# Optimization experiments

Measured on AMD Instinct MI355X. Metric: run time of the kernel, lower is better.

Reference implementation:

```python
import jax, jax.numpy as jnp
import numpy as np

B, N, D, H = 2, 2048, 1024, 16
DH = D // H
SCALE = DH ** -0.5

def setup_inputs() -> dict:
    key = jax.random.key(0)
    k1, k2, k3 = jax.random.split(key, 3)
    x = jax.random.normal(k1, (B, N, D), dtype=jnp.float32)
    W_qkv = jax.random.normal(k2, (3 * D, D), dtype=jnp.float32) * (D ** -0.5)
    W_out = jax.random.normal(k3, (D, D), dtype=jnp.float32) * (D ** -0.5)
    mask = jnp.tril(jnp.ones((N, N), dtype=jnp.int32))  # causal mask; 0 -> -inf
    return {"x": x, "mask": mask, "W_qkv": W_qkv, "W_out": W_out}

def reference(x, mask, W_qkv, W_out):
    b, n, d = x.shape
    qkv = x @ W_qkv.T                                   # [B,N,3D]
    qkv = qkv.reshape(b, n, 3, H, DH).transpose(2, 0, 3, 1, 4)  # [3,B,H,N,DH]
    q, k, v = qkv[0], qkv[1], qkv[2]
    attn = jnp.einsum('bhqd,bhkd->bhqk', q, k) * SCALE  # [B,H,N,N]
    attn = jnp.where(mask == 0, -jnp.inf, attn)
    attn = jax.nn.softmax(attn, axis=-1)
    out = jnp.einsum('bhqk,bhkd->bhqd', attn, v)        # [B,H,N,DH]
    out = out.transpose(0, 2, 1, 3).reshape(b, n, d)    # [B,N,D]
    return out @ W_out.T
```

## Files before the change

### kernel.cpp

```cpp
#include <hip/hip_runtime.h>
#include <hip/hip_bf16.h>


typedef __hip_bfloat16 bf16;
typedef short bf16x8 __attribute__((ext_vector_type(8)));
typedef short bf16x4 __attribute__((ext_vector_type(4)));
typedef float f32x4 __attribute__((ext_vector_type(4)));

#define QSCALE 0.1803368801111204f

typedef __attribute__((address_space(3))) unsigned int lds_u32;
typedef const __attribute__((address_space(1))) unsigned int glob_u32;

__device__ __forceinline__ void glds16(const void* g, void* l) {
    __builtin_amdgcn_global_load_lds((glob_u32*)g, (lds_u32*)l, 16, 0, 0);
}

__device__ __forceinline__ short f2bf(float f) {
    __hip_bfloat16 h = __float2bfloat16(f);
    return *reinterpret_cast<short*>(&h);
}

__device__ __forceinline__ unsigned pack_bf16(float a, float b) {
    unsigned au = __builtin_bit_cast(unsigned, a) + 0x8000u;
    unsigned bu = __builtin_bit_cast(unsigned, b) + 0x8000u;
    return __builtin_amdgcn_perm(bu, au, 0x07060302u);
}

__global__ void cast_all(const float* __restrict__ x, const float* __restrict__ wqkv,
                         const float* __restrict__ wout,
                         bf16* __restrict__ xb, bf16* __restrict__ wqkvb,
                         bf16* __restrict__ woutb) {
    int i = blockIdx.x * blockDim.x + threadIdx.x;
    const float4* s; short4* d; int o;
    if (i < 1048576)               { s = (const float4*)x;    d = (short4*)xb;    o = i; }
    else if (i < 1835008)          { s = (const float4*)wqkv; d = (short4*)wqkvb; o = i - 1048576; }
    else                           { s = (const float4*)wout; d = (short4*)woutb; o = i - 1835008; }
    float4 f = s[o];
    short4 v;
    v.x = f2bf(f.x); v.y = f2bf(f.y); v.z = f2bf(f.z); v.w = f2bf(f.w);
    d[o] = v;
}

__global__ __launch_bounds__(256)
void gemm128_qkv(const bf16* __restrict__ A, const bf16* __restrict__ Bt,
                 bf16* __restrict__ qp, bf16* __restrict__ kp, bf16* __restrict__ vp,
                 int K) {
    __shared__ alignas(16) short As[2][4096];
    __shared__ alignas(16) short Bs[2][4096];

    const int tid = threadIdx.x;
    const int wave = tid >> 6, lane = tid & 63;
    const int quad = lane >> 4, l16 = lane & 15;
    const int wm = wave >> 1, wn = wave & 1;
    const int m0 = blockIdx.x * 128;
    const int n0 = blockIdx.y * 128;

    f32x4 acc[4][4] = {};

    const int srow = tid >> 2;
    const int skk  = (((tid & 3) ^ ((tid >> 3) & 3))) * 8;
    const bf16* Ag = A  + (size_t)(m0 + srow) * K + skk;
    const bf16* Bg = Bt + (size_t)(n0 + srow) * K + skk;
    const size_t rowskip = (size_t)64 * K;
    short* Asl = &As[0][0] + tid * 8;
    short* Bsl = &Bs[0][0] + tid * 8;

    const int xk = (quad ^ ((l16 >> 1) & 3)) * 8;
    const int arow = wm * 64 + l16;
    const int brow = wn * 64 + l16;

    const int KI = K >> 5;
    glds16(Ag, Asl);
    glds16(Ag + rowskip, Asl + 2048);
    glds16(Bg, Bsl);
    glds16(Bg + rowskip, Bsl + 2048);
    __syncthreads();

    int buf = 0;
    for (int ki = 0; ki < KI; ++ki) {
        if (ki + 1 < KI) {
            const bf16* ag = Ag + (ki + 1) * 32;
            const bf16* bg = Bg + (ki + 1) * 32;
            short* ad = Asl + (buf ^ 1) * 4096;
            short* bd = Bsl + (buf ^ 1) * 4096;
            glds16(ag, ad);
            glds16(ag + rowskip, ad + 2048);
            glds16(bg, bd);
            glds16(bg + rowskip, bd + 2048);
        }
        const short* ab = &As[buf][0];
        const short* bb = &Bs[buf][0];
        bf16x8 af[4], bf[4];
        #pragma unroll
        for (int mt = 0; mt < 4; ++mt)
            af[mt] = *reinterpret_cast<const bf16x8*>(ab + (arow + mt * 16) * 32 + xk);
        #pragma unroll
        for (int nt = 0; nt < 4; ++nt)
            bf[nt] = *reinterpret_cast<const bf16x8*>(bb + (brow + nt * 16) * 32 + xk);
        #pragma unroll
        for (int mt = 0; mt < 4; ++mt)
            #pragma unroll
            for (int nt = 0; nt < 4; ++nt)
                acc[mt][nt] = __builtin_amdgcn_mfma_f32_16x16x32_bf16(
                    af[mt], bf[nt], acc[mt][nt], 0, 0, 0);
        __syncthreads();
        buf ^= 1;
    }

    #pragma unroll
    for (int mt = 0; mt < 4; ++mt) {
        #pragma unroll
        for (int nt = 0; nt < 4; ++nt) {
            #pragma unroll
            for (int r = 0; r < 4; ++r) {
                int gm = m0 + wm * 64 + mt * 16 + quad * 4 + r;
                int gn = n0 + wn * 64 + nt * 16 + l16;
                float val = acc[mt][nt][r];
                int sel = gn >> 10, rem = gn & 1023;
                int h = rem >> 6, dh = rem & 63;
                int b = gm >> 11, nq = gm & 2047;
                if (sel == 0) val *= QSCALE;
                bf16* dst = (sel == 0) ? qp : ((sel == 1) ? kp : vp);
                dst[((((size_t)b * 16 + h) * 2048) + nq) * 64 + dh] = __float2bfloat16(val);
            }
        }
    }
}

__global__ __launch_bounds__(256)
void gemm_out(const bf16* __restrict__ A, const bf16* __restrict__ Bt,
              float* __restrict__ Cf, int K, int Ncols) {
    __shared__ alignas(16) short As[2][4096];
    __shared__ alignas(16) short Bs[2][2048];

    const int tid = threadIdx.x;
    const int wave = tid >> 6, lane = tid & 63;
    const int quad = lane >> 4, l16 = lane & 15;
    const int wm = wave >> 1, wn = wave & 1;
    const int m0 = blockIdx.x * 128;
    const int n0 = blockIdx.y * 64;

    f32x4 acc[4][2] = {};

    const int srow = tid >> 2;
    const int skk  = (((tid & 3) ^ ((tid >> 3) & 3))) * 8;
    const bf16* Ag = A  + (size_t)(m0 + srow) * K + skk;
    const bf16* Bg = Bt + (size_t)(n0 + srow) * K + skk;
    const size_t rowskip = (size_t)64 * K;
    short* Asl = &As[0][0] + tid * 8;
    short* Bsl = &Bs[0][0] + tid * 8;

    const int xk = (quad ^ ((l16 >> 1) & 3)) * 8;
    const int arow = wm * 64 + l16;
    const int brow = wn * 32 + l16;

    const int KI = K >> 5;
    glds16(Ag, Asl);
    glds16(Ag + rowskip, Asl + 2048);
    glds16(Bg, Bsl);
    __syncthreads();

    int buf = 0;
    for (int ki = 0; ki < KI; ++ki) {
        if (ki + 1 < KI) {
            const bf16* ag = Ag + (ki + 1) * 32;
            const bf16* bg = Bg + (ki + 1) * 32;
            short* ad = Asl + (buf ^ 1) * 4096;
            short* bd = Bsl + (buf ^ 1) * 2048;
            glds16(ag, ad);
            glds16(ag + rowskip, ad + 2048);
            glds16(bg, bd);
        }
        const short* ab = &As[buf][0];
        const short* bb = &Bs[buf][0];
        bf16x8 af[4], bf[2];
        #pragma unroll
        for (int mt = 0; mt < 4; ++mt)
            af[mt] = *reinterpret_cast<const bf16x8*>(ab + (arow + mt * 16) * 32 + xk);
        #pragma unroll
        for (int nt = 0; nt < 2; ++nt)
            bf[nt] = *reinterpret_cast<const bf16x8*>(bb + (brow + nt * 16) * 32 + xk);
        #pragma unroll
        for (int mt = 0; mt < 4; ++mt)
            #pragma unroll
            for (int nt = 0; nt < 2; ++nt)
                acc[mt][nt] = __builtin_amdgcn_mfma_f32_16x16x32_bf16(
                    af[mt], bf[nt], acc[mt][nt], 0, 0, 0);
        __syncthreads();
        buf ^= 1;
    }

    #pragma unroll
    for (int mt = 0; mt < 4; ++mt) {
        #pragma unroll
        for (int nt = 0; nt < 2; ++nt) {
            #pragma unroll
            for (int r = 0; r < 4; ++r) {
                int gm = m0 + wm * 64 + mt * 16 + quad * 4 + r;
                int gn = n0 + wn * 32 + nt * 16 + l16;
                Cf[(size_t)gm * Ncols + gn] = acc[mt][nt][r];
            }
        }
    }
}

__global__ __launch_bounds__(256, 2)
void flash_attn(const bf16* __restrict__ Q, const bf16* __restrict__ K,
                const bf16* __restrict__ V, bf16* __restrict__ O) {
    __shared__ alignas(16) short Ks[2][128][72];
    __shared__ alignas(16) short Vt[2][64][132];

    const int tid = threadIdx.x;
    const int wave = tid >> 6, lane = tid & 63;
    const int quad = lane >> 4, l16 = lane & 15;
    const int bh = blockIdx.x;
    const int yy = blockIdx.y;
    const int qt = (yy < 8) ? yy : (15 - (yy & 7));
    const int Q0 = qt * 128;
    const float NEG_INF = -__builtin_inff();

    const bf16* Qb = Q + (size_t)bh * 2048 * 64;
    const bf16* Kb = K + (size_t)bh * 2048 * 64;
    const bf16* Vb = V + (size_t)bh * 2048 * 64;

    const int qrowA = Q0 + wave * 16 + l16;
    const int qrowB = qrowA + 64;
    const bf16x8 qfA0 = *reinterpret_cast<const bf16x8*>(Qb + (size_t)qrowA * 64 + quad * 8);
    const bf16x8 qfA1 = *reinterpret_cast<const bf16x8*>(Qb + (size_t)qrowA * 64 + 32 + quad * 8);
    const bf16x8 qfB0 = *reinterpret_cast<const bf16x8*>(Qb + (size_t)qrowB * 64 + quad * 8);
    const bf16x8 qfB1 = *reinterpret_cast<const bf16x8*>(Qb + (size_t)qrowB * 64 + 32 + quad * 8);

    float lA = 0.f, lB = 0.f;
    f32x4 oA[4] = {}, oB[4] = {};

    const int krow = tid >> 2;
    const int kcol = (tid & 3) * 16;
    const int kb   = (tid & 15) * 4;
    const int db   = (tid >> 4) * 4;

    {
        #pragma unroll
        for (int g = 0; g < 2; ++g) {
            const bf16* kr = Kb + (size_t)(g * 64 + krow) * 64 + kcol;
            *reinterpret_cast<bf16x8*>(&Ks[0][g * 64 + krow][kcol])     = *reinterpret_cast<const bf16x8*>(kr);
            *reinterpret_cast<bf16x8*>(&Ks[0][g * 64 + krow][kcol + 8]) = *reinterpret_cast<const bf16x8*>(kr + 8);
        }
        #pragma unroll
        for (int g = 0; g < 2; ++g) {
            const int kbg = g * 64 + kb;
            bf16x4 L0 = *reinterpret_cast<const bf16x4*>(Vb + (size_t)(kbg + 0) * 64 + db);
            bf16x4 L1 = *reinterpret_cast<const bf16x4*>(Vb + (size_t)(kbg + 1) * 64 + db);
            bf16x4 L2 = *reinterpret_cast<const bf16x4*>(Vb + (size_t)(kbg + 2) * 64 + db);
            bf16x4 L3 = *reinterpret_cast<const bf16x4*>(Vb + (size_t)(kbg + 3) * 64 + db);
            #pragma unroll
            for (int j = 0; j < 4; ++j) {
                bf16x4 w; w[0] = L0[j]; w[1] = L1[j]; w[2] = L2[j]; w[3] = L3[j];
                *reinterpret_cast<bf16x4*>(&Vt[0][db + j][kbg]) = w;
            }
        }
    }
    __syncthreads();

    int buf = 0;
    for (int j0 = 0; j0 < Q0; j0 += 128) {
        const bf16* Kn = Kb + (size_t)(j0 + 128) * 64;
        const bf16* Vn = Vb + (size_t)(j0 + 128) * 64;
        bf16x8 nk[2][2];
        bf16x4 NV[2][4];
        #pragma unroll
        for (int g = 0; g < 2; ++g) {
            const bf16* kr = Kn + (size_t)(g * 64 + krow) * 64 + kcol;
            nk[g][0] = *reinterpret_cast<const bf16x8*>(kr);
            nk[g][1] = *reinterpret_cast<const bf16x8*>(kr + 8);
            const int kbg = g * 64 + kb;
            #pragma unroll
            for (int j = 0; j < 4; ++j)
                NV[g][j] = *reinterpret_cast<const bf16x4*>(Vn + (size_t)(kbg + j) * 64 + db);
        }

        bf16x8 kf[8][2];
        #pragma unroll
        for (int t = 0; t < 8; ++t) {
            kf[t][0] = *reinterpret_cast<const bf16x8*>(&Ks[buf][16 * t + l16][quad * 8]);
            kf[t][1] = *reinterpret_cast<const bf16x8*>(&Ks[buf][16 * t + l16][32 + quad * 8]);
        }

        bf16x4 pkA[8], pkB[8];
        f32x4 sA, sB, sAn, sBn;
        {
            __builtin_amdgcn_s_setprio(1);
            sA = {}; sB = {};
            sA = __builtin_amdgcn_mfma_f32_16x16x32_bf16(kf[0][0], qfA0, sA, 0, 0, 0);
            sA = __builtin_amdgcn_mfma_f32_16x16x32_bf16(kf[0][1], qfA1, sA, 0, 0, 0);
            sB = __builtin_amdgcn_mfma_f32_16x16x32_bf16(kf[0][0], qfB0, sB, 0, 0, 0);
            sB = __builtin_amdgcn_mfma_f32_16x16x32_bf16(kf[0][1], qfB1, sB, 0, 0, 0);
            __builtin_amdgcn_s_setprio(0);
        }
        #pragma unroll
        for (int t = 0; t < 8; ++t) {
            if (t < 7) {
                __builtin_amdgcn_s_setprio(1);
                sAn = {}; sBn = {};
                sAn = __builtin_amdgcn_mfma_f32_16x16x32_bf16(kf[t + 1][0], qfA0, sAn, 0, 0, 0);
                sAn = __builtin_amdgcn_mfma_f32_16x16x32_bf16(kf[t + 1][1], qfA1, sAn, 0, 0, 0);
                sBn = __builtin_amdgcn_mfma_f32_16x16x32_bf16(kf[t + 1][0], qfB0, sBn, 0, 0, 0);
                sBn = __builtin_amdgcn_mfma_f32_16x16x32_bf16(kf[t + 1][1], qfB1, sBn, 0, 0, 0);
                __builtin_amdgcn_s_setprio(0);
            }
            float a0 = __builtin_amdgcn_exp2f(sA[0]);
            float a1 = __builtin_amdgcn_exp2f(sA[1]);
            float a2 = __builtin_amdgcn_exp2f(sA[2]);
            float a3 = __builtin_amdgcn_exp2f(sA[3]);
            float b0 = __builtin_amdgcn_exp2f(sB[0]);
            float b1 = __builtin_amdgcn_exp2f(sB[1]);
            float b2 = __builtin_amdgcn_exp2f(sB[2]);
            float b3 = __builtin_amdgcn_exp2f(sB[3]);
            lA += (a0 + a1) + (a2 + a3);
            lB += (b0 + b1) + (b2 + b3);
            unsigned* pa = reinterpret_cast<unsigned*>(&pkA[t]);
            pa[0] = pack_bf16(a0, a1); pa[1] = pack_bf16(a2, a3);
            unsigned* pb = reinterpret_cast<unsigned*>(&pkB[t]);
            pb[0] = pack_bf16(b0, b1); pb[1] = pack_bf16(b2, b3);
            if (t > 0) {
                __builtin_amdgcn_s_setprio(1);
                #pragma unroll
                for (int dt = 0; dt < 4; ++dt) {
                    bf16x4 vf = *reinterpret_cast<const bf16x4*>(
                        &Vt[buf][dt * 16 + l16][(t - 1) * 16 + quad * 4]);
                    oA[dt] = __builtin_amdgcn_mfma_f32_16x16x16bf16_1k(vf, pkA[t - 1], oA[dt], 0, 0, 0);
                    oB[dt] = __builtin_amdgcn_mfma_f32_16x16x16bf16_1k(vf, pkB[t - 1], oB[dt], 0, 0, 0);
                }
                __builtin_amdgcn_s_setprio(0);
            }
            if (t < 7) { sA = sAn; sB = sBn; }
        }

        #pragma unroll
        for (int g = 0; g < 2; ++g) {
            *reinterpret_cast<bf16x8*>(&Ks[buf ^ 1][g * 64 + krow][kcol])     = nk[g][0];
            *reinterpret_cast<bf16x8*>(&Ks[buf ^ 1][g * 64 + krow][kcol + 8]) = nk[g][1];
            const int kbg = g * 64 + kb;
            #pragma unroll
            for (int j = 0; j < 4; ++j) {
                bf16x4 w; w[0] = NV[g][0][j]; w[1] = NV[g][1][j]; w[2] = NV[g][2][j]; w[3] = NV[g][3][j];
                *reinterpret_cast<bf16x4*>(&Vt[buf ^ 1][db + j][kbg]) = w;
            }
        }

        {
            __builtin_amdgcn_s_setprio(1);
            #pragma unroll
            for (int dt = 0; dt < 4; ++dt) {
                bf16x4 vf = *reinterpret_cast<const bf16x4*>(
                    &Vt[buf][dt * 16 + l16][7 * 16 + quad * 4]);
                oA[dt] = __builtin_amdgcn_mfma_f32_16x16x16bf16_1k(vf, pkA[7], oA[dt], 0, 0, 0);
                oB[dt] = __builtin_amdgcn_mfma_f32_16x16x16bf16_1k(vf, pkB[7], oB[dt], 0, 0, 0);
            }
            __builtin_amdgcn_s_setprio(0);
        }
        __syncthreads();
        buf ^= 1;
    }

    {
        bf16x4 pkA[8], pkB[8];
        #pragma unroll
        for (int t = 0; t < 8; ++t) {
            const bool actB = (t <= wave + 4);
            const bool actA = (t <= wave);
            if (actB) {
                bf16x8 k0 = *reinterpret_cast<const bf16x8*>(&Ks[buf][16 * t + l16][quad * 8]);
                bf16x8 k1 = *reinterpret_cast<const bf16x8*>(&Ks[buf][16 * t + l16][32 + quad * 8]);
                f32x4 sB = {};
                sB = __builtin_amdgcn_mfma_f32_16x16x32_bf16(k0, qfB0, sB, 0, 0, 0);
                sB = __builtin_amdgcn_mfma_f32_16x16x32_bf16(k1, qfB1, sB, 0, 0, 0);
                if (t == wave + 4) {
                    #pragma unroll
                    for (int r = 0; r < 4; ++r)
                        if (quad * 4 + r > l16) sB[r] = NEG_INF;
                }
                float b0 = __builtin_amdgcn_exp2f(sB[0]);
                float b1 = __builtin_amdgcn_exp2f(sB[1]);
                float b2 = __builtin_amdgcn_exp2f(sB[2]);
                float b3 = __builtin_amdgcn_exp2f(sB[3]);
                lB += (b0 + b1) + (b2 + b3);
                unsigned* pb = reinterpret_cast<unsigned*>(&pkB[t]);
                pb[0] = pack_bf16(b0, b1); pb[1] = pack_bf16(b2, b3);
                if (actA) {
                    f32x4 sA = {};
                    sA = __builtin_amdgcn_mfma_f32_16x16x32_bf16(k0, qfA0, sA, 0, 0, 0);
                    sA = __builtin_amdgcn_mfma_f32_16x16x32_bf16(k1, qfA1, sA, 0, 0, 0);
                    if (t == wave) {
                        #pragma unroll
                        for (int r = 0; r < 4; ++r)
                            if (quad * 4 + r > l16) sA[r] = NEG_INF;
                    }
                    float a0 = __builtin_amdgcn_exp2f(sA[0]);
                    float a1 = __builtin_amdgcn_exp2f(sA[1]);
                    float a2 = __builtin_amdgcn_exp2f(sA[2]);
                    float a3 = __builtin_amdgcn_exp2f(sA[3]);
                    lA += (a0 + a1) + (a2 + a3);
                    unsigned* pa = reinterpret_cast<unsigned*>(&pkA[t]);
                    pa[0] = pack_bf16(a0, a1); pa[1] = pack_bf16(a2, a3);
                }
            }
        }
        #pragma unroll
        for (int t = 0; t < 8; ++t) {
            if (t <= wave + 4) {
                #pragma unroll
                for (int dt = 0; dt < 4; ++dt) {
                    bf16x4 vf = *reinterpret_cast<const bf16x4*>(
                        &Vt[buf][dt * 16 + l16][t * 16 + quad * 4]);
                    oB[dt] = __builtin_amdgcn_mfma_f32_16x16x16bf16_1k(vf, pkB[t], oB[dt], 0, 0, 0);
                    if (t <= wave)
                        oA[dt] = __builtin_amdgcn_mfma_f32_16x16x16bf16_1k(vf, pkA[t], oA[dt], 0, 0, 0);
                }
            }
        }
    }

    lA += __shfl_xor(lA, 16, 64);
    lA += __shfl_xor(lA, 32, 64);
    lB += __shfl_xor(lB, 16, 64);
    lB += __shfl_xor(lB, 32, 64);
    const float invA = 1.f / lA;
    const float invB = 1.f / lB;

    const int b = bh >> 4, h = bh & 15;
    bf16* orowA = O + ((size_t)b * 2048 + qrowA) * 1024 + h * 64;
    bf16* orowB = O + ((size_t)b * 2048 + qrowB) * 1024 + h * 64;
    #pragma unroll
    for (int dt = 0; dt < 4; ++dt) {
        bf16x4 wA, wB;
        unsigned* ua = reinterpret_cast<unsigned*>(&wA);
        ua[0] = pack_bf16(oA[dt][0] * invA, oA[dt][1] * invA);
        ua[1] = pack_bf16(oA[dt][2] * invA, oA[dt][3] * invA);
        *reinterpret_cast<bf16x4*>(orowA + dt * 16 + quad * 4) = wA;
        unsigned* ub = reinterpret_cast<unsigned*>(&wB);
        ub[0] = pack_bf16(oB[dt][0] * invB, oB[dt][1] * invB);
        ub[1] = pack_bf16(oB[dt][2] * invB, oB[dt][3] * invB);
        *reinterpret_cast<bf16x4*>(orowB + dt * 16 + quad * 4) = wB;
    }
}

extern "C" void kernel_launch(void* const* d_in, const int* in_sizes, int n_in,
                              void* d_out, int out_size, void* d_ws, size_t ws_size,
                              hipStream_t stream) {
    const float* x    = (const float*)d_in[0];
    const float* Wqkv = (const float*)d_in[2];
    const float* Wout = (const float*)d_in[3];
    float* out = (float*)d_out;

    char* ws = (char*)d_ws;
    bf16* x_bf    = (bf16*)(ws);
    bf16* wqkv_bf = (bf16*)(ws + 8388608);
    bf16* wout_bf = (bf16*)(ws + 14680064);
    bf16* q       = (bf16*)(ws + 16777216);
    bf16* k       = (bf16*)(ws + 25165824);
    bf16* v       = (bf16*)(ws + 33554432);
    bf16* ao      = (bf16*)(ws + 41943040);

    cast_all<<<8192, 256, 0, stream>>>(x, Wqkv, Wout, x_bf, wqkv_bf, wout_bf);
    gemm128_qkv<<<dim3(32, 24), 256, 0, stream>>>(x_bf, wqkv_bf, q, k, v, 1024);
    flash_attn<<<dim3(32, 16), 256, 0, stream>>>(q, k, v, ao);
    gemm_out<<<dim3(32, 16), 256, 0, stream>>>(ao, wout_bf, out, 1024, 1024);
}
```

Baseline: 177.8 us.

## Split flash attention along keys into two halves and merge partial outputs

The attention kernel now splits each query tile's key range into two halves over a third grid dimension, processes 64-key tiles with smaller LDS buffers, and writes unnormalised bf16 partial outputs plus row sums. A new merge kernel adds the two partials and divides by the combined sum. This doubles the block count and raises occupancy, with the aim of filling the GPU better and balancing the causal workload. In exchange it adds an extra kernel launch, extra global traffic for the partials, and bf16 rounding of unnormalised accumulators. It also drops the software-pipelined QK/PV interleave of the old main loop.

After: 300.1 us. +68.8%, slower.

```diff
diff --git a/kernel.cpp b/kernel.cpp
--- a/kernel.cpp
+++ b/kernel.cpp
@@ -19,6 +19,10 @@
 __device__ __forceinline__ short f2bf(float f) {
     __hip_bfloat16 h = __float2bfloat16(f);
     return *reinterpret_cast<short*>(&h);
+}
+
+__device__ __forceinline__ float b2f(short s) {
+    return __builtin_bit_cast(float, ((unsigned)(unsigned short)s) << 16);
 }
 
 __device__ __forceinline__ unsigned pack_bf16(float a, float b) {
@@ -205,11 +209,12 @@
     }
 }
 
-__global__ __launch_bounds__(256, 2)
+__global__ __launch_bounds__(256, 4)
 void flash_attn(const bf16* __restrict__ Q, const bf16* __restrict__ K,
-                const bf16* __restrict__ V, bf16* __restrict__ O) {
-    __shared__ alignas(16) short Ks[2][128][72];
-    __shared__ alignas(16) short Vt[2][64][132];
+                const bf16* __restrict__ V, bf16* __restrict__ Opart,
+                float* __restrict__ Lpart) {
+    __shared__ alignas(16) short Ks[2][64][72];
+    __shared__ alignas(16) short Vt[2][64][68];
 
     const int tid = threadIdx.x;
     const int wave = tid >> 6, lane = tid & 63;
@@ -217,7 +222,11 @@
     const int bh = blockIdx.x;
     const int yy = blockIdx.y;
     const int qt = (yy < 8) ? yy : (15 - (yy & 7));
+    const int ksplit = blockIdx.z;
     const int Q0 = qt * 128;
+    const int nst = qt + 1;
+    const int j0_beg = ksplit ? 64 * nst : 0;
+    const int j0_end = ksplit ? 128 * nst : 64 * nst;
     const float NEG_INF = -__builtin_inff();
 
     const bf16* Qb = Q + (size_t)bh * 2048 * 64;
@@ -240,142 +249,55 @@
     const int db   = (tid >> 4) * 4;
 
     {
-        #pragma unroll
-        for (int g = 0; g < 2; ++g) {
-            const bf16* kr = Kb + (size_t)(g * 64 + krow) * 64 + kcol;
-            *reinterpret_cast<bf16x8*>(&Ks[0][g * 64 + krow][kcol])     = *reinterpret_cast<const bf16x8*>(kr);
-            *reinterpret_cast<bf16x8*>(&Ks[0][g * 64 + krow][kcol + 8]) = *reinterpret_cast<const bf16x8*>(kr + 8);
-        }
-        #pragma unroll
-        for (int g = 0; g < 2; ++g) {
-            const int kbg = g * 64 + kb;
-            bf16x4 L0 = *reinterpret_cast<const bf16x4*>(Vb + (size_t)(kbg + 0) * 64 + db);
-            bf16x4 L1 = *reinterpret_cast<const bf16x4*>(Vb + (size_t)(kbg + 1) * 64 + db);
-            bf16x4 L2 = *reinterpret_cast<const bf16x4*>(Vb + (size_t)(kbg + 2) * 64 + db);
-            bf16x4 L3 = *reinterpret_cast<const bf16x4*>(Vb + (size_t)(kbg + 3) * 64 + db);
-            #pragma unroll
-            for (int j = 0; j < 4; ++j) {
-                bf16x4 w; w[0] = L0[j]; w[1] = L1[j]; w[2] = L2[j]; w[3] = L3[j];
-                *reinterpret_cast<bf16x4*>(&Vt[0][db + j][kbg]) = w;
-            }
+        const bf16* K0 = Kb + (size_t)j0_beg * 64;
+        const bf16* V0 = Vb + (size_t)j0_beg * 64;
+        bf16x8 a0 = *reinterpret_cast<const bf16x8*>(K0 + (size_t)krow * 64 + kcol);
+        bf16x8 a1 = *reinterpret_cast<const bf16x8*>(K0 + (size_t)krow * 64 + kcol + 8);
+        bf16x4 L0 = *reinterpret_cast<const bf16x4*>(V0 + (size_t)(kb + 0) * 64 + db);
+        bf16x4 L1 = *reinterpret_cast<const bf16x4*>(V0 + (size_t)(kb + 1) * 64 + db);
+        bf16x4 L2 = *reinterpret_cast<const bf16x4*>(V0 + (size_t)(kb + 2) * 64 + db);
+        bf16x4 L3 = *reinterpret_cast<const bf16x4*>(V0 + (size_t)(kb + 3) * 64 + db);
+        *reinterpret_cast<bf16x8*>(&Ks[0][krow][kcol]) = a0;
+        *reinterpret_cast<bf16x8*>(&Ks[0][krow][kcol + 8]) = a1;
+        #pragma unroll
+        for (int j = 0; j < 4; ++j) {
+            bf16x4 w; w[0] = L0[j]; w[1] = L1[j]; w[2] = L2[j]; w[3] = L3[j];
+            *reinterpret_cast<bf16x4*>(&Vt[0][db + j][kb]) = w;
         }
     }
     __syncthreads();
 
     int buf = 0;
-    for (int j0 = 0; j0 < Q0; j0 += 128) {
-        const bf16* Kn = Kb + (size_t)(j0 + 128) * 64;
-        const bf16* Vn = Vb + (size_t)(j0 + 128) * 64;
-        bf16x8 nk[2][2];
-        bf16x4 NV[2][4];
-        #pragma unroll
-        for (int g = 0; g < 2; ++g) {
-            const bf16* kr = Kn + (size_t)(g * 64 + krow) * 64 + kcol;
-            nk[g][0] = *reinterpret_cast<const bf16x8*>(kr);
-            nk[g][1] = *reinterpret_cast<const bf16x8*>(kr + 8);
-            const int kbg = g * 64 + kb;
-            #pragma unroll
-            for (int j = 0; j < 4; ++j)
-                NV[g][j] = *reinterpret_cast<const bf16x4*>(Vn + (size_t)(kbg + j) * 64 + db);
-        }
-
-        bf16x8 kf[8][2];
-        #pragma unroll
-        for (int t = 0; t < 8; ++t) {
-            kf[t][0] = *reinterpret_cast<const bf16x8*>(&Ks[buf][16 * t + l16][quad * 8]);
-            kf[t][1] = *reinterpret_cast<const bf16x8*>(&Ks[buf][16 * t + l16][32 + quad * 8]);
-        }
-
-        bf16x4 pkA[8], pkB[8];
-        f32x4 sA, sB, sAn, sBn;
-        {
-            __builtin_amdgcn_s_setprio(1);
-            sA = {}; sB = {};
-            sA = __builtin_amdgcn_mfma_f32_16x16x32_bf16(kf[0][0], qfA0, sA, 0, 0, 0);
-            sA = __builtin_amdgcn_mfma_f32_16x16x32_bf16(kf[0][1], qfA1, sA, 0, 0, 0);
-            sB = __builtin_amdgcn_mfma_f32_16x16x32_bf16(kf[0][0], qfB0, sB, 0, 0, 0);
-            sB = __builtin_amdgcn_mfma_f32_16x16x32_bf16(kf[0][1], qfB1, sB, 0, 0, 0);
-            __builtin_amdgcn_s_setprio(0);
-        }
-        #pragma unroll
-        for (int t = 0; t < 8; ++t) {
-            if (t < 7) {
-                __builtin_amdgcn_s_setprio(1);
-                sAn = {}; sBn = {};
-                sAn = __builtin_amdgcn_mfma_f32_16x16x32_bf16(kf[t + 1][0], qfA0, sAn, 0, 0, 0);
-                sAn = __builtin_amdgcn_mfma_f32_16x16x32_bf16(kf[t + 1][1], qfA1, sAn, 0, 0, 0);
-                sBn = __builtin_amdgcn_mfma_f32_16x16x32_bf16(kf[t + 1][0], qfB0, sBn, 0, 0, 0);
-                sBn = __builtin_amdgcn_mfma_f32_16x16x32_bf16(kf[t + 1][1], qfB1, sBn, 0, 0, 0);
-                __builtin_amdgcn_s_setprio(0);
-            }
-            float a0 = __builtin_amdgcn_exp2f(sA[0]);
-            float a1 = __builtin_amdgcn_exp2f(sA[1]);
-            float a2 = __builtin_amdgcn_exp2f(sA[2]);
-            float a3 = __builtin_amdgcn_exp2f(sA[3]);
-            float b0 = __builtin_amdgcn_exp2f(sB[0]);
-            float b1 = __builtin_amdgcn_exp2f(sB[1]);
-            float b2 = __builtin_amdgcn_exp2f(sB[2]);
-            float b3 = __builtin_amdgcn_exp2f(sB[3]);
-            lA += (a0 + a1) + (a2 + a3);
-            lB += (b0 + b1) + (b2 + b3);
-            unsigned* pa = reinterpret_cast<unsigned*>(&pkA[t]);
-            pa[0] = pack_bf16(a0, a1); pa[1] = pack_bf16(a2, a3);
-            unsigned* pb = reinterpret_cast<unsigned*>(&pkB[t]);
-            pb[0] = pack_bf16(b0, b1); pb[1] = pack_bf16(b2, b3);
-            if (t > 0) {
-                __builtin_amdgcn_s_setprio(1);
-                #pragma unroll
-                for (int dt = 0; dt < 4; ++dt) {
-                    bf16x4 vf = *reinterpret_cast<const bf16x4*>(
-                        &Vt[buf][dt * 16 + l16][(t - 1) * 16 + quad * 4]);
-                    oA[dt] = __builtin_amdgcn_mfma_f32_16x16x16bf16_1k(vf, pkA[t - 1], oA[dt], 0, 0, 0);
-                    oB[dt] = __builtin_amdgcn_mfma_f32_16x16x16bf16_1k(vf, pkB[t - 1], oB[dt], 0, 0, 0);
-                }
-                __builtin_amdgcn_s_setprio(0);
-            }
-            if (t < 7) { sA = sAn; sB = sBn; }
-        }
-
-        #pragma unroll
-        for (int g = 0; g < 2; ++g) {
-            *reinterpret_cast<bf16x8*>(&Ks[buf ^ 1][g * 64 + krow][kcol])     = nk[g][0];
-            *reinterpret_cast<bf16x8*>(&Ks[buf ^ 1][g * 64 + krow][kcol + 8]) = nk[g][1];
-            const int kbg = g * 64 + kb;
-            #pragma unroll
-            for (int j = 0; j < 4; ++j) {
-                bf16x4 w; w[0] = NV[g][0][j]; w[1] = NV[g][1][j]; w[2] = NV[g][2][j]; w[3] = NV[g][3][j];
-                *reinterpret_cast<bf16x4*>(&Vt[buf ^ 1][db + j][kbg]) = w;
-            }
-        }
-
-        {
-            __builtin_amdgcn_s_setprio(1);
-            #pragma unroll
-            for (int dt = 0; dt < 4; ++dt) {
-                bf16x4 vf = *reinterpret_cast<const bf16x4*>(
-                    &Vt[buf][dt * 16 + l16][7 * 16 + quad * 4]);
-                oA[dt] = __builtin_amdgcn_mfma_f32_16x16x16bf16_1k(vf, pkA[7], oA[dt], 0, 0, 0);
-                oB[dt] = __builtin_amdgcn_mfma_f32_16x16x16bf16_1k(vf, pkB[7], oB[dt], 0, 0, 0);
-            }
-            __builtin_amdgcn_s_setprio(0);
-        }
-        __syncthreads();
-        buf ^= 1;
-    }
-
-    {
-        bf16x4 pkA[8], pkB[8];
-        #pragma unroll
-        for (int t = 0; t < 8; ++t) {
-            const bool actB = (t <= wave + 4);
-            const bool actA = (t <= wave);
+    for (int j0 = j0_beg; j0 < j0_end; j0 += 64) {
+        const bool pf = (j0 + 64 < j0_end);
+        bf16x8 nk0, nk1;
+        bf16x4 N0, N1, N2, N3;
+        if (pf) {
+            const bf16* Kn = Kb + (size_t)(j0 + 64) * 64;
+            const bf16* Vn = Vb + (size_t)(j0 + 64) * 64;
+            nk0 = *reinterpret_cast<const bf16x8*>(Kn + (size_t)krow * 64 + kcol);
+            nk1 = *reinterpret_cast<const bf16x8*>(Kn + (size_t)krow * 64 + kcol + 8);
+            N0 = *reinterpret_cast<const bf16x4*>(Vn + (size_t)(kb + 0) * 64 + db);
+            N1 = *reinterpret_cast<const bf16x4*>(Vn + (size_t)(kb + 1) * 64 + db);
+            N2 = *reinterpret_cast<const bf16x4*>(Vn + (size_t)(kb + 2) * 64 + db);
+            N3 = *reinterpret_cast<const bf16x4*>(Vn + (size_t)(kb + 3) * 64 + db);
+        }
+
+        const bool d1 = (j0 == Q0);
+        const bool d2 = (j0 > Q0);
+
+        bf16x4 pkA[4], pkB[4];
+        #pragma unroll
+        for (int t = 0; t < 4; ++t) {
+            const bool actB = !d2 || (t <= wave);
+            const bool actA = !d2 && (!d1 || t <= wave);
             if (actB) {
                 bf16x8 k0 = *reinterpret_cast<const bf16x8*>(&Ks[buf][16 * t + l16][quad * 8]);
                 bf16x8 k1 = *reinterpret_cast<const bf16x8*>(&Ks[buf][16 * t + l16][32 + quad * 8]);
                 f32x4 sB = {};
                 sB = __builtin_amdgcn_mfma_f32_16x16x32_bf16(k0, qfB0, sB, 0, 0, 0);
                 sB = __builtin_amdgcn_mfma_f32_16x16x32_bf16(k1, qfB1, sB, 0, 0, 0);
-                if (t == wave + 4) {
+                if (d2 && t == wave) {
                     #pragma unroll
                     for (int r = 0; r < 4; ++r)
                         if (quad * 4 + r > l16) sB[r] = NEG_INF;
@@ -391,7 +313,7 @@
                     f32x4 sA = {};
                     sA = __builtin_amdgcn_mfma_f32_16x16x32_bf16(k0, qfA0, sA, 0, 0, 0);
                     sA = __builtin_amdgcn_mfma_f32_16x16x32_bf16(k1, qfA1, sA, 0, 0, 0);
-                    if (t == wave) {
+                    if (d1 && t == wave) {
                         #pragma unroll
                         for (int r = 0; r < 4; ++r)
                             if (quad * 4 + r > l16) sA[r] = NEG_INF;
@@ -406,43 +328,82 @@
                 }
             }
         }
-        #pragma unroll
-        for (int t = 0; t < 8; ++t) {
-            if (t <= wave + 4) {
+
+        #pragma unroll
+        for (int t = 0; t < 4; ++t) {
+            const bool actB = !d2 || (t <= wave);
+            const bool actA = !d2 && (!d1 || t <= wave);
+            if (actB) {
                 #pragma unroll
                 for (int dt = 0; dt < 4; ++dt) {
                     bf16x4 vf = *reinterpret_cast<const bf16x4*>(
                         &Vt[buf][dt * 16 + l16][t * 16 + quad * 4]);
                     oB[dt] = __builtin_amdgcn_mfma_f32_16x16x16bf16_1k(vf, pkB[t], oB[dt], 0, 0, 0);
-                    if (t <= wave)
+                    if (actA)
                         oA[dt] = __builtin_amdgcn_mfma_f32_16x16x16bf16_1k(vf, pkA[t], oA[dt], 0, 0, 0);
                 }
             }
         }
+
+        if (pf) {
+            *reinterpret_cast<bf16x8*>(&Ks[buf ^ 1][krow][kcol]) = nk0;
+            *reinterpret_cast<bf16x8*>(&Ks[buf ^ 1][krow][kcol + 8]) = nk1;
+            #pragma unroll
+            for (int j = 0; j < 4; ++j) {
+                bf16x4 w; w[0] = N0[j]; w[1] = N1[j]; w[2] = N2[j]; w[3] = N3[j];
+                *reinterpret_cast<bf16x4*>(&Vt[buf ^ 1][db + j][kb]) = w;
+            }
+        }
+        __syncthreads();
+        buf ^= 1;
     }
 
     lA += __shfl_xor(lA, 16, 64);
     lA += __shfl_xor(lA, 32, 64);
     lB += __shfl_xor(lB, 16, 64);
     lB += __shfl_xor(lB, 32, 64);
-    const float invA = 1.f / lA;
-    const float invB = 1.f / lB;
 
     const int b = bh >> 4, h = bh & 15;
-    bf16* orowA = O + ((size_t)b * 2048 + qrowA) * 1024 + h * 64;
-    bf16* orowB = O + ((size_t)b * 2048 + qrowB) * 1024 + h * 64;
+    if (quad == 0) {
+        Lpart[((size_t)ksplit * 32 + bh) * 2048 + qrowA] = lA;
+        Lpart[((size_t)ksplit * 32 + bh) * 2048 + qrowB] = lB;
+    }
+    bf16* orowA = Opart + ((size_t)ksplit * 4096 + b * 2048 + qrowA) * 1024 + h * 64;
+    bf16* orowB = Opart + ((size_t)ksplit * 4096 + b * 2048 + qrowB) * 1024 + h * 64;
     #pragma unroll
     for (int dt = 0; dt < 4; ++dt) {
         bf16x4 wA, wB;
         unsigned* ua = reinterpret_cast<unsigned*>(&wA);
-        ua[0] = pack_bf16(oA[dt][0] * invA, oA[dt][1] * invA);
-        ua[1] = pack_bf16(oA[dt][2] * invA, oA[dt][3] * invA);
+        ua[0] = pack_bf16(oA[dt][0], oA[dt][1]);
+        ua[1] = pack_bf16(oA[dt][2], oA[dt][3]);
         *reinterpret_cast<bf16x4*>(orowA + dt * 16 + quad * 4) = wA;
         unsigned* ub = reinterpret_cast<unsigned*>(&wB);
-        ub[0] = pack_bf16(oB[dt][0] * invB, oB[dt][1] * invB);
-        ub[1] = pack_bf16(oB[dt][2] * invB, oB[dt][3] * invB);
+        ub[0] = pack_bf16(oB[dt][0], oB[dt][1]);
+        ub[1] = pack_bf16(oB[dt][2], oB[dt][3]);
         *reinterpret_cast<bf16x4*>(orowB + dt * 16 + quad * 4) = wB;
     }
+}
+
+__global__ void merge_o(const bf16* __restrict__ Op, const float* __restrict__ Lp,
+                        bf16* __restrict__ ao) {
+    int i = blockIdx.x * blockDim.x + threadIdx.x;
+    int row = i >> 7;
+    int cc  = (i & 127) << 3;
+    int r = row & 2047, b = row >> 11;
+    int bh = b * 16 + (cc >> 6);
+    float l = Lp[(size_t)bh * 2048 + r] + Lp[(size_t)(32 + bh) * 2048 + r];
+    float inv = 1.f / l;
+    bf16x8 o0 = *reinterpret_cast<const bf16x8*>(Op + (size_t)row * 1024 + cc);
+    bf16x8 o1 = *reinterpret_cast<const bf16x8*>(Op + (size_t)(4096 + row) * 1024 + cc);
+    bf16x8 w;
+    unsigned* u = reinterpret_cast<unsigned*>(&w);
+    #pragma unroll
+    for (int j = 0; j < 4; ++j) {
+        float f0 = (b2f(o0[2 * j])     + b2f(o1[2 * j]))     * inv;
+        float f1 = (b2f(o0[2 * j + 1]) + b2f(o1[2 * j + 1])) * inv;
+        u[j] = pack_bf16(f0, f1);
+    }
+    *reinterpret_cast<bf16x8*>(ao + (size_t)row * 1024 + cc) = w;
 }
 
 extern "C" void kernel_launch(void* const* d_in, const int* in_sizes, int n_in,
@@ -461,9 +422,12 @@
     bf16* k       = (bf16*)(ws + 25165824);
     bf16* v       = (bf16*)(ws + 33554432);
     bf16* ao      = (bf16*)(ws + 41943040);
+    bf16* opart   = (bf16*)(ws + 50331648);
+    float* lpart  = (float*)(ws + 67108864);
 
     cast_all<<<8192, 256, 0, stream>>>(x, Wqkv, Wout, x_bf, wqkv_bf, wout_bf);
     gemm128_qkv<<<dim3(32, 24), 256, 0, stream>>>(x_bf, wqkv_bf, q, k, v, 1024);
-    flash_attn<<<dim3(32, 16), 256, 0, stream>>>(q, k, v, ao);
+    flash_attn<<<dim3(32, 16, 2), 256, 0, stream>>>(q, k, v, opart, lpart);
+    merge_o<<<2048, 256, 0, stream>>>(opart, lpart, ao);
     gemm_out<<<dim3(32, 16), 256, 0, stream>>>(ao, wout_bf, out, 1024, 1024);
 }
```
